# Kernel tuning notes

Measured on AMD Instinct MI355X. Metric: run time of the kernel, lower is better.

## Reference

```python
import jax, jax.numpy as jnp
import numpy as np

N = 4_000_000   # points at level d
SIDE = 1024     # coordinate range per axis
HALF = SIDE // 2  # parent coord range


def setup_inputs() -> dict:
    key = jax.random.key(0)
    k1, k2 = jax.random.split(key)
    xyz = jax.random.randint(k1, (N, 3), 0, SIDE, dtype=jnp.int32)
    b = (jnp.arange(N, dtype=jnp.int32) % 4)[:, None]  # 4 batches
    coords = jnp.concatenate([b, xyz], axis=1)          # (N,4): [b,x,y,z]
    kernel = jnp.ones((8,), dtype=jnp.float32)          # frozen all-ones 2x2x2 conv weights
    return {"coords": coords, "kernel": kernel}


def _fog(coords, kernel):
    # pos(): occupancy code 2**(x%2 + 2*y%2 + 4*z%2)
    bits = coords[:, 1:4] & 1                       # (N,3)
    off = bits[:, 0] + 2 * bits[:, 1] + 4 * bits[:, 2]  # (N,) child offset in 2x2x2 window
    pos = jnp.exp2(off.astype(jnp.float32))         # (N,) code in {1,2,4,...,128}
    contrib = pos * kernel[off]                     # per-offset conv weight (all ones)
    # stride-2 conv: parent voxel = floor(xyz/2); linearize (b,z,y,x) into a key
    parent = coords[:, 1:4] >> 1                    # (N,3)
    keys = (((coords[:, 0].astype(jnp.int64) * HALF + parent[:, 2]) * HALF
             + parent[:, 1]) * HALF + parent[:, 0])
    ukeys, inv = jnp.unique(keys, return_inverse=True, size=N, fill_value=-1)
    feats = jax.ops.segment_sum(contrib, inv, num_segments=N)[:, None]  # (N,1)
    # decode padded unique keys back to coords; pad slots -> -1
    px = (ukeys % HALF).astype(jnp.int32)
    py = ((ukeys // HALF) % HALF).astype(jnp.int32)
    pz = ((ukeys // (HALF * HALF)) % HALF).astype(jnp.int32)
    pb = (ukeys // (HALF * HALF * HALF)).astype(jnp.int32)
    valid = (ukeys >= 0)[:, None]
    coords_out = jnp.where(valid, jnp.stack([pb, px, py, pz], axis=1), -1)
    return coords_out, feats


def reference(coords, kernel):
    return _fog(coords, kernel)
```

## Files before the change

### kernel.cpp

```cpp
#include <hip/hip_runtime.h>
#include <stdint.h>

typedef unsigned int u32;
typedef unsigned long long u64;

#define LBITS  14
#define LMASK  ((1u << LBITS) - 1u)
#define NBUCK  (1u << (29 - LBITS))
#define BWORDS (1u << (LBITS - 5))
#define WPL    (BWORDS / 64)
#define WOPAD  (BWORDS + BWORDS / 32)
#define FCAP   192
#define BPB    4
#define TILE_A 4096
#define RPT    (TILE_A / 256)
#define CCAP   16384
#define S2     4
#define CAP2   4608
#define RPT2   (CAP2 / 256)
#define RECV   4
#define CAP    224
#define SCAN_ELEM 2048

__device__ __forceinline__ u32 woidx(u32 w) { return w + (w >> 5); }

__device__ __forceinline__ void wsync() {
    asm volatile("s_waitcnt lgkmcnt(0)" ::: "memory");
}

__device__ __forceinline__ u32 make_key(int4 c) {
    return ((((u32)c.x * 512u + ((u32)c.w >> 1)) * 512u + ((u32)c.z >> 1)) * 512u)
           + ((u32)c.y >> 1);
}

__global__ void zero1(u32* __restrict__ p, u32 g) {
    u32 i = blockIdx.x * 256u + threadIdx.x;
    if (i < g) p[i] = 0u;
}

__global__ void __launch_bounds__(256) part1f(const int4* __restrict__ coords,
        u32* __restrict__ ccur, u32* __restrict__ tmp,
        u32* __restrict__ cursor, int n) {
    __shared__ u32 stage[TILE_A];
    __shared__ u32 lcur[256];
    __shared__ u32 gb[256];
    __shared__ u32 wtot[4];
    u32 t = threadIdx.x, wave = t >> 6, lane = t & 63u;
    if (blockIdx.x < 128u) cursor[blockIdx.x * 256u + t] = 0u;
    u32 base = blockIdx.x * TILE_A;
    u32 m = min((u32)TILE_A, (u32)n - base);
    lcur[t] = 0u;
    __syncthreads();
    u32 recv[RPT];
    #pragma unroll
    for (int k = 0; k < RPT; ++k) {
        u32 j = (u32)k * 256u + t;
        if (j < m) {
            int4 c = coords[base + j];
            u32 key = make_key(c);
            u32 off = ((u32)c.y & 1u) | (((u32)c.z & 1u) << 1) | (((u32)c.w & 1u) << 2);
            u32 rec = (key << 3) | off;
            recv[k] = rec;
            atomicAdd(&lcur[rec >> 24], 1u);
        }
    }
    __syncthreads();
    u32 v = lcur[t];
    u32 incl = v;
    #pragma unroll
    for (int d = 1; d < 64; d <<= 1) {
        u32 x = __shfl_up(incl, d);
        if ((int)lane >= d) incl += x;
    }
    if (lane == 63u) wtot[wave] = incl;
    __syncthreads();
    u32 off = (wave > 0u ? wtot[0] : 0u) + (wave > 1u ? wtot[1] : 0u)
            + (wave > 2u ? wtot[2] : 0u);
    u32 excl = off + incl - v;
    u32 gbase = atomicAdd(&ccur[t * 16u], v);
    lcur[t] = excl;
    gb[t] = (t << 14) + gbase - excl;
    __syncthreads();
    #pragma unroll
    for (int k = 0; k < RPT; ++k) {
        u32 j = (u32)k * 256u + t;
        if (j < m) {
            u32 rec = recv[k];
            u32 pos = atomicAdd(&lcur[rec >> 24], 1u);
            stage[pos] = rec;
        }
    }
    __syncthreads();
    for (u32 j = t; j < m; j += 256u) {
        u32 rec = stage[j];
        tmp[gb[rec >> 24] + j] = rec;
    }
}

__global__ void scan_reduce(const u32* __restrict__ data, u32* __restrict__ partial, u32 G) {
    __shared__ u32 s[256];
    u32 t = threadIdx.x;
    u32 base = blockIdx.x * SCAN_ELEM + t * 8u;
    u32 sum = 0;
    #pragma unroll
    for (int j = 0; j < 8; ++j) { u32 idx = base + j; if (idx < G) sum += data[idx]; }
    s[t] = sum; __syncthreads();
    for (int d = 128; d > 0; d >>= 1) { if ((int)t < d) s[t] += s[t + d]; __syncthreads(); }
    if (t == 0) partial[blockIdx.x] = s[0];
}

__global__ void scan_apply2(const u32* __restrict__ data, u32* __restrict__ out,
                            const u32* __restrict__ partial, u32 G, u32 NB,
                            u32* __restrict__ total) {
    __shared__ u32 s[256];
    __shared__ u32 pb[2];
    u32 t = threadIdx.x;
    u32 p = (t < NB) ? partial[t] : 0u;
    u32 pbef = (t < blockIdx.x) ? p : 0u;
    s[t] = pbef; __syncthreads();
    for (int d = 128; d > 0; d >>= 1) { if ((int)t < d) s[t] += s[t + d]; __syncthreads(); }
    if (t == 0) pb[0] = s[0];
    __syncthreads();
    if (total) {
        s[t] = p; __syncthreads();
        for (int d = 128; d > 0; d >>= 1) { if ((int)t < d) s[t] += s[t + d]; __syncthreads(); }
        if (t == 0) pb[1] = s[0];
        __syncthreads();
        if (blockIdx.x == NB - 1u && t == 0u) total[0] = pb[1];
    }
    u32 base = blockIdx.x * SCAN_ELEM + t * 8u;
    u32 v[8]; u32 sum = 0;
    #pragma unroll
    for (int j = 0; j < 8; ++j) {
        u32 idx = base + j;
        v[j] = (idx < G) ? data[idx] : 0u;
        sum += v[j];
    }
    s[t] = sum; __syncthreads();
    for (int d = 1; d < 256; d <<= 1) {
        u32 add = (t >= (u32)d) ? s[t - d] : 0u;
        __syncthreads(); s[t] += add; __syncthreads();
    }
    u32 run = s[t] - sum + pb[0];
    #pragma unroll
    for (int j = 0; j < 8; ++j) {
        u32 idx = base + j;
        if (idx < G) { u32 x = v[j]; out[idx] = run; run += x; }
    }
}

__global__ void __launch_bounds__(256) part2(const u32* __restrict__ tmp,
        const u32* __restrict__ ccur, u32* __restrict__ cursor,
        u32* __restrict__ buckrec, int n) {
    __shared__ u32 stage[CAP2];
    __shared__ u32 lcur[128];
    __shared__ u32 dstb[128];
    __shared__ u32 wtot[2];
    u32 t = threadIdx.x, lane = t & 63u;
    u32 c = blockIdx.x / S2, s = blockIdx.x % S2;
    u32 cs = c << 14;
    u32 L = ccur[c * 16u];
    u32 lo = cs + L * s / S2, hi = cs + L * (s + 1u) / S2;
    u32 cnt = hi - lo;
    if (cnt <= (u32)CAP2) {
        if (t < 128u) lcur[t] = 0u;
        __syncthreads();
        u32 recv[RPT2];
        #pragma unroll
        for (int k = 0; k < RPT2; ++k) {
            u32 j = (u32)k * 256u + t;
            if (j < cnt) {
                u32 rec = tmp[lo + j];
                recv[k] = rec;
                atomicAdd(&lcur[(rec >> 17) & 127u], 1u);
            }
        }
        __syncthreads();
        u32 v = 0, incl = 0;
        if (t < 128u) {
            v = lcur[t];
            incl = v;
            #pragma unroll
            for (int d = 1; d < 64; d <<= 1) {
                u32 x = __shfl_up(incl, d);
                if ((int)lane >= d) incl += x;
            }
            if (lane == 63u) wtot[t >> 6] = incl;
        }
        __syncthreads();
        if (t < 128u) {
            u32 off = (t >= 64u) ? wtot[0] : 0u;
            u32 excl = off + incl - v;
            u32 bucket = (c << 7) | t;
            u32 gbase = atomicAdd(&cursor[bucket], v);
            lcur[t] = excl;
            dstb[t] = bucket * (u32)CAP + gbase - excl;
        }
        __syncthreads();
        #pragma unroll
        for (int k = 0; k < RPT2; ++k) {
            u32 j = (u32)k * 256u + t;
            if (j < cnt) {
                u32 rec = recv[k];
                u32 pos = atomicAdd(&lcur[(rec >> 17) & 127u], 1u);
                stage[pos] = rec;
            }
        }
        __syncthreads();
        for (u32 j = t; j < cnt; j += 256u) {
            u32 rec = stage[j];
            buckrec[dstb[(rec >> 17) & 127u] + j] = rec;
        }
    } else {
        for (u32 i = lo + t; i < hi; i += 256u) {
            u32 rec = tmp[i];
            u32 b = rec >> 17;
            u32 pos = atomicAdd(&cursor[b], 1u);
            buckrec[b * (u32)CAP + pos] = rec;
        }
    }
}

__global__ void __launch_bounds__(256) pass_count(const u32* __restrict__ buckrec,
        const u32* __restrict__ bcnt, u32* __restrict__ ucount, int n) {
    __shared__ u32 bm[BPB][WOPAD];
    u32 wave = threadIdx.x >> 6, lane = threadIdx.x & 63u;
    u32 bucket = blockIdx.x * BPB + wave;
    u32* B = bm[wave];
    #pragma unroll
    for (int j = 0; j < WPL; ++j) B[woidx(lane * WPL + j)] = 0u;
    wsync();
    u32 start = bucket * (u32)CAP;
    u32 end = start + bcnt[bucket];
    for (u32 i = start + lane; i < end; i += 64u) {
        u32 lk = (buckrec[i] >> 3) & LMASK;
        atomicOr(&B[woidx(lk >> 5)], 1u << (lk & 31u));
    }
    wsync();
    u32 sum = 0;
    #pragma unroll
    for (int j = 0; j < WPL; ++j) sum += __popc(B[woidx(lane * WPL + j)]);
    #pragma unroll
    for (int d = 1; d < 64; d <<= 1) sum += __shfl_xor(sum, d);
    if (lane == 0u) ucount[bucket] = sum;
}

__global__ void __launch_bounds__(256) pass_emit(const u32* __restrict__ buckrec,
        const u32* __restrict__ bcnt, const u32* __restrict__ ubase,
        const float* __restrict__ kern, float4* __restrict__ rows,
        float* __restrict__ feats, int n) {
    __shared__ u32 bm[BPB][WOPAD];
    __shared__ u32 wofW[BPB][BWORDS];
    __shared__ float fl[BPB][FCAP];
    __shared__ float ksc[BPB][8];
    u32 wave = threadIdx.x >> 6, lane = threadIdx.x & 63u;
    u32 bucket = blockIdx.x * BPB + wave;
    u32* B = bm[wave];
    u32* W = wofW[wave];
    float* F = fl[wave];
    #pragma unroll
    for (int j = 0; j < WPL; ++j) B[woidx(lane * WPL + j)] = 0u;
    #pragma unroll
    for (u32 j = lane; j < FCAP; j += 64u) F[j] = 0.f;
    if (lane < 8u) ksc[wave][lane] = (float)(1u << lane) * kern[lane];
    wsync();
    u32 start = bucket * (u32)CAP;
    u32 cnt = bcnt[bucket];
    u32 recv[RECV];
    #pragma unroll
    for (int k = 0; k < RECV; ++k) {
        u32 idx = (u32)k * 64u + lane;
        if (idx < cnt) {
            u32 rec = buckrec[start + idx];
            recv[k] = rec;
            u32 lk = (rec >> 3) & LMASK;
            atomicOr(&B[woidx(lk >> 5)], 1u << (lk & 31u));
        }
    }
    wsync();
    u32 wv[WPL]; u32 pc[WPL]; u32 sum = 0;
    #pragma unroll
    for (int j = 0; j < WPL; ++j) {
        wv[j] = B[woidx(lane * WPL + j)];
        pc[j] = __popc(wv[j]);
        sum += pc[j];
    }
    u32 incl = sum;
    #pragma unroll
    for (int d = 1; d < 64; d <<= 1) {
        u32 tt = __shfl_up(incl, d);
        if ((int)lane >= d) incl += tt;
    }
    u32 lex = incl - sum;
    u32 uc = __shfl(incl, 63);
    {
        u32 r = lex;
        #pragma unroll
        for (int j = 0; j < WPL; ++j) { W[((u32)j << 6) | lane] = r; r += pc[j]; }
    }
    wsync();
    u32 base = ubase[bucket];
    bool lds_ok = (uc <= FCAP);
    if (!lds_ok) {
        for (u32 j = lane; j < uc; j += 64u) feats[base + j] = 0.f;
        asm volatile("s_waitcnt vmcnt(0)" ::: "memory");
    }
    #pragma unroll
    for (int k = 0; k < RECV; ++k) {
        u32 idx = (u32)k * 64u + lane;
        if (idx < cnt) {
            u32 rec = recv[k];
            float contrib = ksc[wave][rec & 7u];
            u32 lk = (rec >> 3) & LMASK;
            u32 w = lk >> 5, bit = lk & 31u;
            u32 r = W[((w & 7u) << 6) | (w >> 3)]
                  + __popc(B[woidx(w)] & ((1u << bit) - 1u));
            if (lds_ok) atomicAdd(&F[r], contrib);
            else        atomicAdd(&feats[base + r], contrib);
        }
    }
    wsync();
    u32 rank = base + lex;
    u32 keyhi = bucket << LBITS;
    #pragma unroll
    for (int j = 0; j < WPL; ++j) {
        u32 bits = wv[j];
        u32 kb = keyhi | ((lane * (u32)WPL + (u32)j) << 5);
        while (bits) {
            u32 tz = __builtin_ctz(bits);
            bits &= bits - 1u;
            u32 key = kb | tz;
            rows[rank++] = make_float4((float)(key >> 27), (float)(key & 511u),
                                       (float)((key >> 9) & 511u),
                                       (float)((key >> 18) & 511u));
        }
    }
    if (lds_ok) {
        for (u32 j = lane; j < uc; j += 64u) feats[base + j] = F[j];
    }
}

__global__ void pad_fill(float4* __restrict__ rows, float* __restrict__ feats,
                         const u32* __restrict__ counter, int n) {
    int i = blockIdx.x * blockDim.x + threadIdx.x;
    if (i < n && (u32)i >= counter[0]) {
        rows[i] = make_float4(-1.f, -1.f, -1.f, -1.f);
        feats[i] = 0.f;
    }
}

extern "C" void kernel_launch(void* const* d_in, const int* in_sizes, int n_in,
                              void* d_out, int out_size, void* d_ws, size_t ws_size,
                              hipStream_t stream) {
    const int n = in_sizes[0] / 4;
    const int4* coords = (const int4*)d_in[0];
    const float* kern  = (const float*)d_in[1];
    const u32 NT = ((u32)n + TILE_A - 1) / TILE_A;
    const u32 NB3 = (NBUCK + SCAN_ELEM - 1) / SCAN_ELEM;

    u32* wsp = (u32*)d_ws;
    u32* tmp     = wsp;
    u32* ccur    = tmp + 256 * CCAP;
    u32* cursor  = ccur + 256 * 16;
    u32* ucount  = cursor + NBUCK;
    u32* ubase   = ucount + NBUCK;
    u32* counter = ubase + NBUCK;
    u32* spart   = counter + 4;
    u32* buckrec = spart + 256;

    float4* rows  = (float4*)d_out;
    float*  feats = (float*)((char*)d_out + (size_t)n * 16);

    zero1<<<16, 256, 0, stream>>>(ccur, 256 * 16);
    part1f<<<NT, 256, 0, stream>>>(coords, ccur, tmp, cursor, n);
    part2<<<256 * S2, 256, 0, stream>>>(tmp, ccur, cursor, buckrec, n);
    pass_count<<<NBUCK / BPB, 256, 0, stream>>>(buckrec, cursor, ucount, n);
    scan_reduce<<<NB3, 256, 0, stream>>>(ucount, spart, NBUCK);
    scan_apply2<<<NB3, 256, 0, stream>>>(ucount, ubase, spart, NBUCK, NB3, counter);
    pass_emit<<<NBUCK / BPB, 256, 0, stream>>>(buckrec, cursor, ubase, kern,
                                               rows, feats, n);
    pad_fill<<<((u32)n + 255) / 256, 256, 0, stream>>>(rows, feats, counter, n);
}
```

Before: 213.8 us.

## Replace two-pass LDS-staged radix partition with direct atomic bucket scatter

Drops the two-level partition (per-tile histogram and LDS staging into coarse chunks, then a second pass splitting into fine buckets). Each point is now scattered straight into its fine bucket through a global atomic on a cursor padded to 16 words per bucket to avoid false sharing. This removes one full read/write pass over the records and a kernel launch. In exchange it issues one global atomic per point and makes uncoalesced scattered writes, and the padded cursor array is larger to zero and to read.

Result: slower. 345.5 us (+61.5%).

```diff
diff --git a/kernel.cpp b/kernel.cpp
--- a/kernel.cpp
+++ b/kernel.cpp
@@ -12,15 +12,11 @@
 #define WOPAD  (BWORDS + BWORDS / 32)
 #define FCAP   192
 #define BPB    4
-#define TILE_A 4096
-#define RPT    (TILE_A / 256)
-#define CCAP   16384
-#define S2     4
-#define CAP2   4608
-#define RPT2   (CAP2 / 256)
 #define RECV   4
 #define CAP    224
+#define CPAD   16
 #define SCAN_ELEM 2048
+#define SBLK   2048
 
 __device__ __forceinline__ u32 woidx(u32 w) { return w + (w >> 5); }
 
@@ -33,67 +29,22 @@
            + ((u32)c.y >> 1);
 }
 
-__global__ void zero1(u32* __restrict__ p, u32 g) {
+__global__ void zero_cur(u32* __restrict__ p, u32 g) {
     u32 i = blockIdx.x * 256u + threadIdx.x;
     if (i < g) p[i] = 0u;
 }
 
-__global__ void __launch_bounds__(256) part1f(const int4* __restrict__ coords,
-        u32* __restrict__ ccur, u32* __restrict__ tmp,
-        u32* __restrict__ cursor, int n) {
-    __shared__ u32 stage[TILE_A];
-    __shared__ u32 lcur[256];
-    __shared__ u32 gb[256];
-    __shared__ u32 wtot[4];
-    u32 t = threadIdx.x, wave = t >> 6, lane = t & 63u;
-    if (blockIdx.x < 128u) cursor[blockIdx.x * 256u + t] = 0u;
-    u32 base = blockIdx.x * TILE_A;
-    u32 m = min((u32)TILE_A, (u32)n - base);
-    lcur[t] = 0u;
-    __syncthreads();
-    u32 recv[RPT];
-    #pragma unroll
-    for (int k = 0; k < RPT; ++k) {
-        u32 j = (u32)k * 256u + t;
-        if (j < m) {
-            int4 c = coords[base + j];
-            u32 key = make_key(c);
-            u32 off = ((u32)c.y & 1u) | (((u32)c.z & 1u) << 1) | (((u32)c.w & 1u) << 2);
-            u32 rec = (key << 3) | off;
-            recv[k] = rec;
-            atomicAdd(&lcur[rec >> 24], 1u);
-        }
-    }
-    __syncthreads();
-    u32 v = lcur[t];
-    u32 incl = v;
-    #pragma unroll
-    for (int d = 1; d < 64; d <<= 1) {
-        u32 x = __shfl_up(incl, d);
-        if ((int)lane >= d) incl += x;
-    }
-    if (lane == 63u) wtot[wave] = incl;
-    __syncthreads();
-    u32 off = (wave > 0u ? wtot[0] : 0u) + (wave > 1u ? wtot[1] : 0u)
-            + (wave > 2u ? wtot[2] : 0u);
-    u32 excl = off + incl - v;
-    u32 gbase = atomicAdd(&ccur[t * 16u], v);
-    lcur[t] = excl;
-    gb[t] = (t << 14) + gbase - excl;
-    __syncthreads();
-    #pragma unroll
-    for (int k = 0; k < RPT; ++k) {
-        u32 j = (u32)k * 256u + t;
-        if (j < m) {
-            u32 rec = recv[k];
-            u32 pos = atomicAdd(&lcur[rec >> 24], 1u);
-            stage[pos] = rec;
-        }
-    }
-    __syncthreads();
-    for (u32 j = t; j < m; j += 256u) {
-        u32 rec = stage[j];
-        tmp[gb[rec >> 24] + j] = rec;
+__global__ void __launch_bounds__(256) scatter(const int4* __restrict__ coords,
+        u32* __restrict__ cursor, u32* __restrict__ buckrec, int n) {
+    u32 stride = SBLK * 256u;
+    for (u32 i = blockIdx.x * 256u + threadIdx.x; i < (u32)n; i += stride) {
+        int4 c = coords[i];
+        u32 key = make_key(c);
+        u32 off = ((u32)c.y & 1u) | (((u32)c.z & 1u) << 1) | (((u32)c.w & 1u) << 2);
+        u32 rec = (key << 3) | off;
+        u32 b = rec >> 17;
+        u32 pos = atomicAdd(&cursor[b * CPAD], 1u);
+        buckrec[b * (u32)CAP + pos] = rec;
     }
 }
 
@@ -149,80 +100,8 @@
     }
 }
 
-__global__ void __launch_bounds__(256) part2(const u32* __restrict__ tmp,
-        const u32* __restrict__ ccur, u32* __restrict__ cursor,
-        u32* __restrict__ buckrec, int n) {
-    __shared__ u32 stage[CAP2];
-    __shared__ u32 lcur[128];
-    __shared__ u32 dstb[128];
-    __shared__ u32 wtot[2];
-    u32 t = threadIdx.x, lane = t & 63u;
-    u32 c = blockIdx.x / S2, s = blockIdx.x % S2;
-    u32 cs = c << 14;
-    u32 L = ccur[c * 16u];
-    u32 lo = cs + L * s / S2, hi = cs + L * (s + 1u) / S2;
-    u32 cnt = hi - lo;
-    if (cnt <= (u32)CAP2) {
-        if (t < 128u) lcur[t] = 0u;
-        __syncthreads();
-        u32 recv[RPT2];
-        #pragma unroll
-        for (int k = 0; k < RPT2; ++k) {
-            u32 j = (u32)k * 256u + t;
-            if (j < cnt) {
-                u32 rec = tmp[lo + j];
-                recv[k] = rec;
-                atomicAdd(&lcur[(rec >> 17) & 127u], 1u);
-            }
-        }
-        __syncthreads();
-        u32 v = 0, incl = 0;
-        if (t < 128u) {
-            v = lcur[t];
-            incl = v;
-            #pragma unroll
-            for (int d = 1; d < 64; d <<= 1) {
-                u32 x = __shfl_up(incl, d);
-                if ((int)lane >= d) incl += x;
-            }
-            if (lane == 63u) wtot[t >> 6] = incl;
-        }
-        __syncthreads();
-        if (t < 128u) {
-            u32 off = (t >= 64u) ? wtot[0] : 0u;
-            u32 excl = off + incl - v;
-            u32 bucket = (c << 7) | t;
-            u32 gbase = atomicAdd(&cursor[bucket], v);
-            lcur[t] = excl;
-            dstb[t] = bucket * (u32)CAP + gbase - excl;
-        }
-        __syncthreads();
-        #pragma unroll
-        for (int k = 0; k < RPT2; ++k) {
-            u32 j = (u32)k * 256u + t;
-            if (j < cnt) {
-                u32 rec = recv[k];
-                u32 pos = atomicAdd(&lcur[(rec >> 17) & 127u], 1u);
-                stage[pos] = rec;
-            }
-        }
-        __syncthreads();
-        for (u32 j = t; j < cnt; j += 256u) {
-            u32 rec = stage[j];
-            buckrec[dstb[(rec >> 17) & 127u] + j] = rec;
-        }
-    } else {
-        for (u32 i = lo + t; i < hi; i += 256u) {
-            u32 rec = tmp[i];
-            u32 b = rec >> 17;
-            u32 pos = atomicAdd(&cursor[b], 1u);
-            buckrec[b * (u32)CAP + pos] = rec;
-        }
-    }
-}
-
 __global__ void __launch_bounds__(256) pass_count(const u32* __restrict__ buckrec,
-        const u32* __restrict__ bcnt, u32* __restrict__ ucount, int n) {
+        const u32* __restrict__ cursor, u32* __restrict__ ucount, int n) {
     __shared__ u32 bm[BPB][WOPAD];
     u32 wave = threadIdx.x >> 6, lane = threadIdx.x & 63u;
     u32 bucket = blockIdx.x * BPB + wave;
@@ -231,7 +110,7 @@
     for (int j = 0; j < WPL; ++j) B[woidx(lane * WPL + j)] = 0u;
     wsync();
     u32 start = bucket * (u32)CAP;
-    u32 end = start + bcnt[bucket];
+    u32 end = start + cursor[bucket * CPAD];
     for (u32 i = start + lane; i < end; i += 64u) {
         u32 lk = (buckrec[i] >> 3) & LMASK;
         atomicOr(&B[woidx(lk >> 5)], 1u << (lk & 31u));
@@ -246,7 +125,7 @@
 }
 
 __global__ void __launch_bounds__(256) pass_emit(const u32* __restrict__ buckrec,
-        const u32* __restrict__ bcnt, const u32* __restrict__ ubase,
+        const u32* __restrict__ cursor, const u32* __restrict__ ubase,
         const float* __restrict__ kern, float4* __restrict__ rows,
         float* __restrict__ feats, int n) {
     __shared__ u32 bm[BPB][WOPAD];
@@ -265,7 +144,7 @@
     if (lane < 8u) ksc[wave][lane] = (float)(1u << lane) * kern[lane];
     wsync();
     u32 start = bucket * (u32)CAP;
-    u32 cnt = bcnt[bucket];
+    u32 cnt = cursor[bucket * CPAD];
     u32 recv[RECV];
     #pragma unroll
     for (int k = 0; k < RECV; ++k) {
@@ -355,14 +234,12 @@
     const int n = in_sizes[0] / 4;
     const int4* coords = (const int4*)d_in[0];
     const float* kern  = (const float*)d_in[1];
-    const u32 NT = ((u32)n + TILE_A - 1) / TILE_A;
     const u32 NB3 = (NBUCK + SCAN_ELEM - 1) / SCAN_ELEM;
+    const u32 CG = NBUCK * CPAD;
 
     u32* wsp = (u32*)d_ws;
-    u32* tmp     = wsp;
-    u32* ccur    = tmp + 256 * CCAP;
-    u32* cursor  = ccur + 256 * 16;
-    u32* ucount  = cursor + NBUCK;
+    u32* cursor  = wsp;
+    u32* ucount  = cursor + CG;
     u32* ubase   = ucount + NBUCK;
     u32* counter = ubase + NBUCK;
     u32* spart   = counter + 4;
@@ -371,9 +248,8 @@
     float4* rows  = (float4*)d_out;
     float*  feats = (float*)((char*)d_out + (size_t)n * 16);
 
-    zero1<<<16, 256, 0, stream>>>(ccur, 256 * 16);
-    part1f<<<NT, 256, 0, stream>>>(coords, ccur, tmp, cursor, n);
-    part2<<<256 * S2, 256, 0, stream>>>(tmp, ccur, cursor, buckrec, n);
+    zero_cur<<<(CG + 255) / 256, 256, 0, stream>>>(cursor, CG);
+    scatter<<<SBLK, 256, 0, stream>>>(coords, cursor, buckrec, n);
     pass_count<<<NBUCK / BPB, 256, 0, stream>>>(buckrec, cursor, ucount, n);
     scan_reduce<<<NB3, 256, 0, stream>>>(ucount, spart, NBUCK);
     scan_apply2<<<NB3, 256, 0, stream>>>(ucount, ubase, spart, NBUCK, NB3, counter);
```

## Fuse second partition pass with unique-count pass using in-place per-chunk LDS sort

Applied to the files above, without the earlier changes.

Replaces the multi-block second radix partition and the separate pass_count kernel with one 1024-thread block per coarse chunk. Each block histograms, sorts the chunk into 128 sub-buckets in LDS, writes it back in place, and counts uniques per sub-bucket straight from LDS. Dense bucket starts and counts replace the fixed-capacity padded bucket array and its global atomics. This removes a global round trip and one launch, at the cost of only 256 large blocks with heavy LDS use, which lowers parallelism and occupancy.

Result: faster. 206.7 us (-3.4%).

```diff
diff --git a/kernel.cpp b/kernel.cpp
--- a/kernel.cpp
+++ b/kernel.cpp
@@ -15,11 +15,9 @@
 #define TILE_A 4096
 #define RPT    (TILE_A / 256)
 #define CCAP   16384
-#define S2     4
-#define CAP2   4608
-#define RPT2   (CAP2 / 256)
+#define P2T    1024
+#define RPT2U  (CCAP / P2T)
 #define RECV   4
-#define CAP    224
 #define SCAN_ELEM 2048
 
 __device__ __forceinline__ u32 woidx(u32 w) { return w + (w >> 5); }
@@ -39,14 +37,12 @@
 }
 
 __global__ void __launch_bounds__(256) part1f(const int4* __restrict__ coords,
-        u32* __restrict__ ccur, u32* __restrict__ tmp,
-        u32* __restrict__ cursor, int n) {
+        u32* __restrict__ ccur, u32* __restrict__ tmp, int n) {
     __shared__ u32 stage[TILE_A];
     __shared__ u32 lcur[256];
     __shared__ u32 gb[256];
     __shared__ u32 wtot[4];
     u32 t = threadIdx.x, wave = t >> 6, lane = t & 63u;
-    if (blockIdx.x < 128u) cursor[blockIdx.x * 256u + t] = 0u;
     u32 base = blockIdx.x * TILE_A;
     u32 m = min((u32)TILE_A, (u32)n - base);
     lcur[t] = 0u;
@@ -94,6 +90,90 @@
     for (u32 j = t; j < m; j += 256u) {
         u32 rec = stage[j];
         tmp[gb[rec >> 24] + j] = rec;
+    }
+}
+
+__global__ void __launch_bounds__(P2T) part2u(u32* __restrict__ tmp,
+        const u32* __restrict__ ccur, u32* __restrict__ cstart,
+        u32* __restrict__ bcnt, u32* __restrict__ ucount) {
+    __shared__ u32 stage[CCAP];
+    __shared__ u32 h[4][128];
+    __shared__ u32 lstart[128];
+    __shared__ u32 lcur[128];
+    __shared__ u32 cnts[128];
+    __shared__ u32 wtot[2];
+    __shared__ u32 bm[16][WOPAD];
+    u32 t = threadIdx.x, wave = t >> 6, lane = t & 63u;
+    u32 c = blockIdx.x;
+    u32 base = c << 14;
+    u32 L = ccur[c * 16u];
+    if (t < 512u) h[t >> 7][t & 127u] = 0u;
+    __syncthreads();
+    u32 recv[RPT2U];
+    u32 hrep = wave & 3u;
+    #pragma unroll
+    for (int k = 0; k < RPT2U; ++k) {
+        u32 j = (u32)k * P2T + t;
+        if (j < L) {
+            u32 rec = tmp[base + j];
+            recv[k] = rec;
+            atomicAdd(&h[hrep][(rec >> 17) & 127u], 1u);
+        }
+    }
+    __syncthreads();
+    u32 v = 0, incl = 0;
+    if (t < 128u) {
+        v = h[0][t] + h[1][t] + h[2][t] + h[3][t];
+        incl = v;
+        #pragma unroll
+        for (int d = 1; d < 64; d <<= 1) {
+            u32 x = __shfl_up(incl, d);
+            if ((int)lane >= d) incl += x;
+        }
+        if (lane == 63u) wtot[t >> 6] = incl;
+    }
+    __syncthreads();
+    if (t < 128u) {
+        u32 off = (t >= 64u) ? wtot[0] : 0u;
+        u32 excl = off + incl - v;
+        lstart[t] = excl;
+        lcur[t] = excl;
+        cnts[t] = v;
+        u32 bucket = (c << 7) | t;
+        cstart[bucket] = base + excl;
+        bcnt[bucket] = v;
+    }
+    __syncthreads();
+    #pragma unroll
+    for (int k = 0; k < RPT2U; ++k) {
+        u32 j = (u32)k * P2T + t;
+        if (j < L) {
+            u32 rec = recv[k];
+            u32 pos = atomicAdd(&lcur[(rec >> 17) & 127u], 1u);
+            stage[pos] = rec;
+        }
+    }
+    __syncthreads();
+    for (u32 j = t; j < L; j += P2T) tmp[base + j] = stage[j];
+    u32* B = bm[wave];
+    for (u32 bi = 0; bi < 8u; ++bi) {
+        u32 b = wave * 8u + bi;
+        #pragma unroll
+        for (int j = 0; j < WPL; ++j) B[woidx(lane * WPL + j)] = 0u;
+        wsync();
+        u32 s0 = lstart[b], cnt = cnts[b];
+        for (u32 i = s0 + lane; i < s0 + cnt; i += 64u) {
+            u32 lk = (stage[i] >> 3) & LMASK;
+            atomicOr(&B[woidx(lk >> 5)], 1u << (lk & 31u));
+        }
+        wsync();
+        u32 sum = 0;
+        #pragma unroll
+        for (int j = 0; j < WPL; ++j) sum += __popc(B[woidx(lane * WPL + j)]);
+        #pragma unroll
+        for (int d = 1; d < 64; d <<= 1) sum += __shfl_xor(sum, d);
+        if (lane == 0u) ucount[(c << 7) | b] = sum;
+        wsync();
     }
 }
 
@@ -149,106 +229,10 @@
     }
 }
 
-__global__ void __launch_bounds__(256) part2(const u32* __restrict__ tmp,
-        const u32* __restrict__ ccur, u32* __restrict__ cursor,
-        u32* __restrict__ buckrec, int n) {
-    __shared__ u32 stage[CAP2];
-    __shared__ u32 lcur[128];
-    __shared__ u32 dstb[128];
-    __shared__ u32 wtot[2];
-    u32 t = threadIdx.x, lane = t & 63u;
-    u32 c = blockIdx.x / S2, s = blockIdx.x % S2;
-    u32 cs = c << 14;
-    u32 L = ccur[c * 16u];
-    u32 lo = cs + L * s / S2, hi = cs + L * (s + 1u) / S2;
-    u32 cnt = hi - lo;
-    if (cnt <= (u32)CAP2) {
-        if (t < 128u) lcur[t] = 0u;
-        __syncthreads();
-        u32 recv[RPT2];
-        #pragma unroll
-        for (int k = 0; k < RPT2; ++k) {
-            u32 j = (u32)k * 256u + t;
-            if (j < cnt) {
-                u32 rec = tmp[lo + j];
-                recv[k] = rec;
-                atomicAdd(&lcur[(rec >> 17) & 127u], 1u);
-            }
-        }
-        __syncthreads();
-        u32 v = 0, incl = 0;
-        if (t < 128u) {
-            v = lcur[t];
-            incl = v;
-            #pragma unroll
-            for (int d = 1; d < 64; d <<= 1) {
-                u32 x = __shfl_up(incl, d);
-                if ((int)lane >= d) incl += x;
-            }
-            if (lane == 63u) wtot[t >> 6] = incl;
-        }
-        __syncthreads();
-        if (t < 128u) {
-            u32 off = (t >= 64u) ? wtot[0] : 0u;
-            u32 excl = off + incl - v;
-            u32 bucket = (c << 7) | t;
-            u32 gbase = atomicAdd(&cursor[bucket], v);
-            lcur[t] = excl;
-            dstb[t] = bucket * (u32)CAP + gbase - excl;
-        }
-        __syncthreads();
-        #pragma unroll
-        for (int k = 0; k < RPT2; ++k) {
-            u32 j = (u32)k * 256u + t;
-            if (j < cnt) {
-                u32 rec = recv[k];
-                u32 pos = atomicAdd(&lcur[(rec >> 17) & 127u], 1u);
-                stage[pos] = rec;
-            }
-        }
-        __syncthreads();
-        for (u32 j = t; j < cnt; j += 256u) {
-            u32 rec = stage[j];
-            buckrec[dstb[(rec >> 17) & 127u] + j] = rec;
-        }
-    } else {
-        for (u32 i = lo + t; i < hi; i += 256u) {
-            u32 rec = tmp[i];
-            u32 b = rec >> 17;
-            u32 pos = atomicAdd(&cursor[b], 1u);
-            buckrec[b * (u32)CAP + pos] = rec;
-        }
-    }
-}
-
-__global__ void __launch_bounds__(256) pass_count(const u32* __restrict__ buckrec,
-        const u32* __restrict__ bcnt, u32* __restrict__ ucount, int n) {
-    __shared__ u32 bm[BPB][WOPAD];
-    u32 wave = threadIdx.x >> 6, lane = threadIdx.x & 63u;
-    u32 bucket = blockIdx.x * BPB + wave;
-    u32* B = bm[wave];
-    #pragma unroll
-    for (int j = 0; j < WPL; ++j) B[woidx(lane * WPL + j)] = 0u;
-    wsync();
-    u32 start = bucket * (u32)CAP;
-    u32 end = start + bcnt[bucket];
-    for (u32 i = start + lane; i < end; i += 64u) {
-        u32 lk = (buckrec[i] >> 3) & LMASK;
-        atomicOr(&B[woidx(lk >> 5)], 1u << (lk & 31u));
-    }
-    wsync();
-    u32 sum = 0;
-    #pragma unroll
-    for (int j = 0; j < WPL; ++j) sum += __popc(B[woidx(lane * WPL + j)]);
-    #pragma unroll
-    for (int d = 1; d < 64; d <<= 1) sum += __shfl_xor(sum, d);
-    if (lane == 0u) ucount[bucket] = sum;
-}
-
 __global__ void __launch_bounds__(256) pass_emit(const u32* __restrict__ buckrec,
-        const u32* __restrict__ bcnt, const u32* __restrict__ ubase,
-        const float* __restrict__ kern, float4* __restrict__ rows,
-        float* __restrict__ feats, int n) {
+        const u32* __restrict__ cstart, const u32* __restrict__ bcnt,
+        const u32* __restrict__ ubase, const float* __restrict__ kern,
+        float4* __restrict__ rows, float* __restrict__ feats, int n) {
     __shared__ u32 bm[BPB][WOPAD];
     __shared__ u32 wofW[BPB][BWORDS];
     __shared__ float fl[BPB][FCAP];
@@ -264,7 +248,7 @@
     for (u32 j = lane; j < FCAP; j += 64u) F[j] = 0.f;
     if (lane < 8u) ksc[wave][lane] = (float)(1u << lane) * kern[lane];
     wsync();
-    u32 start = bucket * (u32)CAP;
+    u32 start = cstart[bucket];
     u32 cnt = bcnt[bucket];
     u32 recv[RECV];
     #pragma unroll
@@ -361,23 +345,22 @@
     u32* wsp = (u32*)d_ws;
     u32* tmp     = wsp;
     u32* ccur    = tmp + 256 * CCAP;
-    u32* cursor  = ccur + 256 * 16;
-    u32* ucount  = cursor + NBUCK;
+    u32* cstart  = ccur + 256 * 16;
+    u32* bcnt    = cstart + NBUCK;
+    u32* ucount  = bcnt + NBUCK;
     u32* ubase   = ucount + NBUCK;
     u32* counter = ubase + NBUCK;
     u32* spart   = counter + 4;
-    u32* buckrec = spart + 256;
 
     float4* rows  = (float4*)d_out;
     float*  feats = (float*)((char*)d_out + (size_t)n * 16);
 
     zero1<<<16, 256, 0, stream>>>(ccur, 256 * 16);
-    part1f<<<NT, 256, 0, stream>>>(coords, ccur, tmp, cursor, n);
-    part2<<<256 * S2, 256, 0, stream>>>(tmp, ccur, cursor, buckrec, n);
-    pass_count<<<NBUCK / BPB, 256, 0, stream>>>(buckrec, cursor, ucount, n);
+    part1f<<<NT, 256, 0, stream>>>(coords, ccur, tmp, n);
+    part2u<<<256, P2T, 0, stream>>>(tmp, ccur, cstart, bcnt, ucount);
     scan_reduce<<<NB3, 256, 0, stream>>>(ucount, spart, NBUCK);
     scan_apply2<<<NB3, 256, 0, stream>>>(ucount, ubase, spart, NBUCK, NB3, counter);
-    pass_emit<<<NBUCK / BPB, 256, 0, stream>>>(buckrec, cursor, ubase, kern,
+    pass_emit<<<NBUCK / BPB, 256, 0, stream>>>(tmp, cstart, bcnt, ubase, kern,
                                                rows, feats, n);
     pad_fill<<<((u32)n + 255) / 256, 256, 0, stream>>>(rows, feats, counter, n);
 }
```
